# Performance work log

Hardware: AMD Instinct MI355X
Metric: run time of the kernel (lower is better)

The kernel has to match this reference:

```python
import jax, jax.numpy as jnp
import numpy as np

VOCAB, D_MODEL, D_STATE, D_CONV, EXPAND = 32000, 1024, 16, 4, 2
D_INNER = EXPAND * D_MODEL          # 2048
DT_RANK = (D_MODEL + 15) // 16      # 64
B, L = 2, 2048


def setup_inputs() -> dict:
    key = jax.random.key(0)
    ks = jax.random.split(key, 13)
    s = 0.02
    return {
        "tokens": jax.random.randint(ks[0], (B, L), 0, VOCAB, dtype=jnp.int32),
        "emb": jax.random.normal(ks[1], (VOCAB, D_MODEL), jnp.float32) * s,
        "in_proj_w": jax.random.normal(ks[2], (2 * D_INNER, D_MODEL), jnp.float32) * s,
        "conv_w": jax.random.normal(ks[3], (D_INNER, D_CONV), jnp.float32) * s,
        "conv_b": jnp.zeros((D_INNER,), jnp.float32),
        "x_proj_w": jax.random.normal(ks[4], (DT_RANK + 2 * D_STATE, D_INNER), jnp.float32) * s,
        "dt_proj_w": jax.random.normal(ks[5], (D_INNER, DT_RANK), jnp.float32) * s,
        "dt_proj_b": jax.random.normal(ks[6], (D_INNER,), jnp.float32) * 0.1,
        "A_log": jnp.log(jnp.broadcast_to(jnp.arange(1, D_STATE + 1, dtype=jnp.float32), (D_INNER, D_STATE))),
        "D": jnp.ones((D_INNER,), jnp.float32),
        "out_proj_w": jax.random.normal(ks[7], (D_MODEL, D_INNER), jnp.float32) * s,
        "head_w": jax.random.normal(ks[8], (VOCAB, D_MODEL), jnp.float32) * s,
        "head_b": jnp.zeros((VOCAB,), jnp.float32),
    }


def _silu(x):
    return x * jax.nn.sigmoid(x)


def _causal_dw_conv(x, w, b):
    # x: [B, L, D], w: [D, K] depthwise causal conv
    K = w.shape[1]
    Ln = x.shape[1]
    xp = jnp.pad(x, ((0, 0), (K - 1, 0), (0, 0)))
    out = b
    for k in range(K):
        out = out + xp[:, k:k + Ln, :] * w[:, k]
    return out


def _mamba_forward(tokens, emb, in_proj_w, conv_w, conv_b, x_proj_w,
                   dt_proj_w, dt_proj_b, A_log, D, out_proj_w, head_w, head_b):
    u = emb[tokens]                                        # [B, L, d_model]
    xz = jnp.einsum('bld,ed->ble', u, in_proj_w)           # [B, L, 2*d_inner]
    x, z = jnp.split(xz, 2, axis=-1)                       # each [B, L, d_inner]
    x = _silu(_causal_dw_conv(x, conv_w, conv_b))

    x_dbl = jnp.einsum('bld,ed->ble', x, x_proj_w)         # [B, L, dt_rank+2*d_state]
    dt, Bm, Cm = jnp.split(x_dbl, [DT_RANK, DT_RANK + D_STATE], axis=-1)
    dt = jax.nn.softplus(jnp.einsum('blr,dr->bld', dt, dt_proj_w) + dt_proj_b)  # [B, L, d_inner]

    A = -jnp.exp(A_log)                                    # [d_inner, d_state]

    # scan over time; per-step inputs in [L, B, ...] layout
    xs = (jnp.swapaxes(dt, 0, 1), jnp.swapaxes(Bm, 0, 1),
          jnp.swapaxes(Cm, 0, 1), jnp.swapaxes(x, 0, 1))

    def step(h, inp):
        dt_t, B_t, C_t, x_t = inp                          # [B,d_inner],[B,d_state],[B,d_state],[B,d_inner]
        dA = jnp.exp(dt_t[:, :, None] * A)                 # [B, d_inner, d_state]
        dBx = dt_t[:, :, None] * B_t[:, None, :] * x_t[:, :, None]
        h = dA * h + dBx
        y_t = jnp.einsum('bds,bs->bd', h, C_t)
        return h, y_t

    h0 = jnp.zeros((B, D_INNER, D_STATE), jnp.float32)
    _, ys = jax.lax.scan(step, h0, xs)                     # ys: [L, B, d_inner]
    y = jnp.swapaxes(ys, 0, 1) + D * x                     # [B, L, d_inner]
    y = y * _silu(z)
    out = jnp.einsum('ble,de->bld', y, out_proj_w)         # [B, L, d_model]
    logits = jnp.einsum('bld,vd->blv', out, head_w) + head_b
    return logits


def reference(tokens, emb, in_proj_w, conv_w, conv_b, x_proj_w,
              dt_proj_w, dt_proj_b, A_log, D, out_proj_w, head_w, head_b):
    return _mamba_forward(tokens, emb, in_proj_w, conv_w, conv_b, x_proj_w,
                          dt_proj_w, dt_proj_b, A_log, D, out_proj_w, head_w, head_b)
```

## Files before the change

kernel.cpp:

```cpp
#include <hip/hip_runtime.h>
#include <hip/hip_bf16.h>
#include <math.h>

#define LOG2E 1.44269504088896340736f

typedef __bf16 bf16x8 __attribute__((ext_vector_type(8)));
typedef float floatx4 __attribute__((ext_vector_type(4)));

static constexpr int VOCAB = 32000, D_MODEL = 1024, D_STATE = 16;
static constexpr int D_INNER = 2048, DT_RANK = 64, NB = 2, LSEQ = 2048;
static constexpr int NTOK = NB * LSEQ;
static constexpr int CL = 64, NCHUNK = LSEQ / CL;

__device__ __forceinline__ unsigned short f2bf(float f) {
    union { __hip_bfloat16 h; unsigned short u; } v;
    v.h = __float2bfloat16(f);
    return v.u;
}

__global__ void embed_kernel(const int* __restrict__ tok, const float* __restrict__ emb,
                             unsigned short* __restrict__ ubf) {
    int g = blockIdx.x * blockDim.x + threadIdx.x;
    int row = g >> 8;
    int c4 = (g & 255) * 4;
    if (row >= NTOK) return;
    int t = tok[row];
    float4 v = *(const float4*)(emb + (size_t)t * D_MODEL + c4);
    ushort4 o;
    o.x = f2bf(v.x); o.y = f2bf(v.y); o.z = f2bf(v.z); o.w = f2bf(v.w);
    *(ushort4*)(ubf + (size_t)row * D_MODEL + c4) = o;
}

__global__ void cvt_kernel(const float* __restrict__ in, unsigned short* __restrict__ out, int n4) {
    int g = blockIdx.x * blockDim.x + threadIdx.x;
    if (g >= n4) return;
    float4 v = ((const float4*)in)[g];
    ushort4 o;
    o.x = f2bf(v.x); o.y = f2bf(v.y); o.z = f2bf(v.z); o.w = f2bf(v.w);
    ((ushort4*)out)[g] = o;
}

__global__ void conv_silu_kernel(const float* __restrict__ xz, const float* __restrict__ cw,
                                 const float* __restrict__ cb, float* __restrict__ xf,
                                 unsigned short* __restrict__ xbf) {
    int g = blockIdx.x * blockDim.x + threadIdx.x;
    if (g >= NTOK * D_INNER) return;
    int d = g & (D_INNER - 1);
    int row = g >> 11;
    int l = row & (LSEQ - 1);
    float w0 = cw[d * 4 + 0], w1 = cw[d * 4 + 1], w2 = cw[d * 4 + 2], w3 = cw[d * 4 + 3];
    const float* xin = xz + (size_t)row * (2 * D_INNER) + d;
    const ptrdiff_t S = 2 * D_INNER;
    float acc = cb[d] + xin[0] * w3;
    if (l >= 1) acc += xin[-S] * w2;
    if (l >= 2) acc += xin[-2 * S] * w1;
    if (l >= 3) acc += xin[-3 * S] * w0;
    float sig = 1.f / (1.f + __builtin_amdgcn_exp2f(-acc * LOG2E));
    float v = acc * sig;
    xf[g] = v;
    xbf[g] = f2bf(v);
}

__global__ void dtin_kernel(const float* __restrict__ xdbl, unsigned short* __restrict__ dtin) {
    int g = blockIdx.x * blockDim.x + threadIdx.x;
    if (g >= NTOK * DT_RANK) return;
    int row = g >> 6, r = g & 63;
    dtin[g] = f2bf(xdbl[(size_t)row * 96 + r]);
}

__global__ void As_kernel(const float* __restrict__ A_log, float* __restrict__ As, int n) {
    int g = blockIdx.x * blockDim.x + threadIdx.x;
    if (g >= n) return;
    As[g] = -__builtin_amdgcn_exp2f(A_log[g] * LOG2E) * LOG2E;
}


__global__ void scan_part1(const float* __restrict__ dt, const float* __restrict__ x,
                           const float* __restrict__ xdbl, const float* __restrict__ As,
                           float* __restrict__ Pc, float* __restrict__ Hc) {
    int g = blockIdx.x * blockDim.x + threadIdx.x;
    int s = g & 15;
    int d = (g >> 4) & (D_INNER - 1);
    int c = (g >> 15) & (NCHUNK - 1);
    int b = g >> 20;
    float a2 = As[d * 16 + s];
    int row0 = b * LSEQ + c * CL;
    const float* dtp = dt + (size_t)row0 * D_INNER + d;
    const float* xp = x + (size_t)row0 * D_INNER + d;
    const float* bp = xdbl + (size_t)row0 * 96 + 64 + s;
    float h = 0.f, esum = 0.f;
    for (int l = 0; l < CL; ++l) {
        float dtv = dtp[(size_t)l * D_INNER];
        float xv = xp[(size_t)l * D_INNER];
        float Bv = bp[(size_t)l * 96];
        float e = dtv * a2;
        esum += e;
        float dA = __builtin_amdgcn_exp2f(e);
        h = dA * h + dtv * Bv * xv;
    }
    Pc[g] = __builtin_amdgcn_exp2f(esum);
    Hc[g] = h;
}

__global__ void scan_combine(const float* __restrict__ Pc, const float* __restrict__ Hc,
                             float* __restrict__ Hinit) {
    int g = blockIdx.x * blockDim.x + threadIdx.x;
    int ds = g & (D_INNER * D_STATE - 1);
    int b = g >> 15;
    size_t base = (size_t)b * NCHUNK * D_INNER * D_STATE + ds;
    float h = 0.f;
    for (int c = 0; c < NCHUNK; ++c) {
        size_t idx = base + (size_t)c * (D_INNER * D_STATE);
        Hinit[idx] = h;
        h = Pc[idx] * h + Hc[idx];
    }
}

__global__ void scan_part2(const float* __restrict__ dt, const float* __restrict__ x,
                           const float* __restrict__ xdbl, const float* __restrict__ xz,
                           const float* __restrict__ As, const float* __restrict__ Dvec,
                           const float* __restrict__ Hinit, unsigned short* __restrict__ ybf) {
    int g = blockIdx.x * blockDim.x + threadIdx.x;
    int s = g & 15;
    int d = (g >> 4) & (D_INNER - 1);
    int c = (g >> 15) & (NCHUNK - 1);
    int b = g >> 20;
    float a2 = As[d * 16 + s];
    float Dv = Dvec[d];
    int row0 = b * LSEQ + c * CL;
    const float* dtp = dt + (size_t)row0 * D_INNER + d;
    const float* xp = x + (size_t)row0 * D_INNER + d;
    const float* bp = xdbl + (size_t)row0 * 96 + 64 + s;
    const float* cp = xdbl + (size_t)row0 * 96 + 80 + s;
    const float* zp = xz + (size_t)row0 * 2 * D_INNER + D_INNER + d;
    unsigned short* yp = ybf + (size_t)row0 * D_INNER + d;
    float h = Hinit[g];
    for (int l = 0; l < CL; ++l) {
        float dtv = dtp[(size_t)l * D_INNER];
        float xv = xp[(size_t)l * D_INNER];
        float Bv = bp[(size_t)l * 96];
        float Cv = cp[(size_t)l * 96];
        float dA = __builtin_amdgcn_exp2f(dtv * a2);
        h = dA * h + dtv * Bv * xv;
        float p = h * Cv;
        p += __shfl_xor(p, 1);
        p += __shfl_xor(p, 2);
        p += __shfl_xor(p, 4);
        p += __shfl_xor(p, 8);
        if (s == 0) {
            float zv = zp[(size_t)l * 2 * D_INNER];
            float sig = 1.f / (1.f + __builtin_amdgcn_exp2f(-zv * LOG2E));
            float y = (p + Dv * xv) * (zv * sig);
            yp[(size_t)l * D_INNER] = f2bf(y);
        }
    }
}

__global__ __launch_bounds__(256, 2)
void gemm_bf16(const unsigned short* __restrict__ A, const unsigned short* __restrict__ Bw,
               float* __restrict__ Cf, unsigned short* __restrict__ Cb,
               const float* __restrict__ bias, int M, int N, int K, int epi) {
    constexpr int BM = 128, BN = 128, BK = 32, LDT = 40;
    __shared__ __align__(16) unsigned short lA[BM * LDT];
    __shared__ __align__(16) unsigned short lB[BN * LDT];
    int tid = threadIdx.x;
    int wave = tid >> 6, lane = tid & 63;
    int quad = lane >> 4, l16 = lane & 15;
    int wr = wave >> 1, wc = wave & 1;
    int m0 = blockIdx.y * BM, n0 = blockIdx.x * BN;

    floatx4 acc[4][4] = {};

    int r0 = tid >> 2, ch = tid & 3;
    int bn0 = n0 + r0; if (bn0 >= N) bn0 = N - 1;
    int bn1 = n0 + r0 + 64; if (bn1 >= N) bn1 = N - 1;
    const int nK = K / BK;
    for (int kt = 0; kt < nK; ++kt) {
        int k0 = kt * BK + ch * 8;
        uint4 va0 = *(const uint4*)(A + (size_t)(m0 + r0) * K + k0);
        uint4 va1 = *(const uint4*)(A + (size_t)(m0 + r0 + 64) * K + k0);
        uint4 vb0 = *(const uint4*)(Bw + (size_t)bn0 * K + k0);
        uint4 vb1 = *(const uint4*)(Bw + (size_t)bn1 * K + k0);
        __syncthreads();
        *(uint4*)&lA[r0 * LDT + ch * 8] = va0;
        *(uint4*)&lA[(r0 + 64) * LDT + ch * 8] = va1;
        *(uint4*)&lB[r0 * LDT + ch * 8] = vb0;
        *(uint4*)&lB[(r0 + 64) * LDT + ch * 8] = vb1;
        __syncthreads();
        bf16x8 af[4], bfr[4];
#pragma unroll
        for (int t = 0; t < 4; ++t) {
            af[t] = *(const bf16x8*)&lA[(wr * 64 + t * 16 + l16) * LDT + quad * 8];
            bfr[t] = *(const bf16x8*)&lB[(wc * 64 + t * 16 + l16) * LDT + quad * 8];
        }
#pragma unroll
        for (int mt = 0; mt < 4; ++mt)
#pragma unroll
            for (int nt = 0; nt < 4; ++nt)
                acc[mt][nt] = __builtin_amdgcn_mfma_f32_16x16x32_bf16(af[mt], bfr[nt], acc[mt][nt], 0, 0, 0);
    }
#pragma unroll
    for (int mt = 0; mt < 4; ++mt) {
#pragma unroll
        for (int nt = 0; nt < 4; ++nt) {
            int col = n0 + wc * 64 + nt * 16 + l16;
            if (col >= N) continue;
            float bv = (epi == 1 || epi == 2) ? bias[col] : 0.f;
#pragma unroll
            for (int r = 0; r < 4; ++r) {
                int row = m0 + wr * 64 + mt * 16 + quad * 4 + r;
                float v = acc[mt][nt][r] + bv;
                if (epi == 1) v = (v > 20.f) ? v : log1pf(__builtin_amdgcn_exp2f(v * LOG2E));
                if (epi == 3) Cb[(size_t)row * N + col] = f2bf(v);
                else Cf[(size_t)row * N + col] = v;
            }
        }
    }
}

extern "C" void kernel_launch(void* const* d_in, const int* in_sizes, int n_in,
                              void* d_out, int out_size, void* d_ws, size_t ws_size,
                              hipStream_t stream) {
    (void)in_sizes; (void)n_in; (void)out_size; (void)ws_size;
    const int* tokens = (const int*)d_in[0];
    const float* emb = (const float*)d_in[1];
    const float* in_proj_w = (const float*)d_in[2];
    const float* conv_w = (const float*)d_in[3];
    const float* conv_b = (const float*)d_in[4];
    const float* x_proj_w = (const float*)d_in[5];
    const float* dt_proj_w = (const float*)d_in[6];
    const float* dt_proj_b = (const float*)d_in[7];
    const float* A_log = (const float*)d_in[8];
    const float* Dvec = (const float*)d_in[9];
    const float* out_proj_w = (const float*)d_in[10];
    const float* head_w = (const float*)d_in[11];
    const float* head_b = (const float*)d_in[12];
    float* logits = (float*)d_out;

    char* ws = (char*)d_ws;
    size_t off = 0;
    auto alloc = [&](size_t bytes) -> void* {
        void* p = ws + off;
        off = (off + bytes + 255) & ~(size_t)255;
        return p;
    };
    unsigned short* u_bf = (unsigned short*)alloc((size_t)NTOK * D_MODEL * 2);
    unsigned short* Win_bf = (unsigned short*)alloc((size_t)2 * D_INNER * D_MODEL * 2);
    float* xz = (float*)alloc((size_t)NTOK * 2 * D_INNER * 4);
    float* xf = (float*)alloc((size_t)NTOK * D_INNER * 4);
    unsigned short* x_bf = (unsigned short*)alloc((size_t)NTOK * D_INNER * 2);
    unsigned short* Wxp_bf = (unsigned short*)alloc((size_t)96 * D_INNER * 2);
    float* xdbl = (float*)alloc((size_t)NTOK * 96 * 4);
    unsigned short* dtin_bf = (unsigned short*)alloc((size_t)NTOK * DT_RANK * 2);
    unsigned short* Wdt_bf = (unsigned short*)alloc((size_t)D_INNER * DT_RANK * 2);
    float* dtf = (float*)alloc((size_t)NTOK * D_INNER * 4);
    float* As = (float*)alloc((size_t)D_INNER * D_STATE * 4);
    unsigned short* y_bf = (unsigned short*)alloc((size_t)NTOK * D_INNER * 2);
    unsigned short* Wout_bf = (unsigned short*)alloc((size_t)D_MODEL * D_INNER * 2);
    unsigned short* out_bf = (unsigned short*)alloc((size_t)NTOK * D_MODEL * 2);
    float* Hinit = (float*)alloc((size_t)NB * NCHUNK * D_INNER * D_STATE * 4);
    unsigned short* Whead_bf = (unsigned short*)xz;
    float* Pc = (float*)u_bf;
    float* Hc = (float*)Win_bf;

    dim3 blk(256);

    embed_kernel<<<dim3(NTOK * D_MODEL / 4 / 256), blk, 0, stream>>>(tokens, emb, u_bf);
    cvt_kernel<<<dim3(2 * D_INNER * D_MODEL / 4 / 256), blk, 0, stream>>>(in_proj_w, Win_bf, 2 * D_INNER * D_MODEL / 4);
    gemm_bf16<<<dim3(2 * D_INNER / 128, NTOK / 128), blk, 0, stream>>>(
        u_bf, Win_bf, xz, nullptr, nullptr, NTOK, 2 * D_INNER, D_MODEL, 0);
    conv_silu_kernel<<<dim3(NTOK * D_INNER / 256), blk, 0, stream>>>(xz, conv_w, conv_b, xf, x_bf);
    cvt_kernel<<<dim3((96 * D_INNER / 4 + 255) / 256), blk, 0, stream>>>(x_proj_w, Wxp_bf, 96 * D_INNER / 4);
    gemm_bf16<<<dim3(1, NTOK / 128), blk, 0, stream>>>(
        x_bf, Wxp_bf, xdbl, nullptr, nullptr, NTOK, 96, D_INNER, 0);
    dtin_kernel<<<dim3(NTOK * DT_RANK / 256), blk, 0, stream>>>(xdbl, dtin_bf);
    cvt_kernel<<<dim3((D_INNER * DT_RANK / 4 + 255) / 256), blk, 0, stream>>>(dt_proj_w, Wdt_bf, D_INNER * DT_RANK / 4);
    gemm_bf16<<<dim3(D_INNER / 128, NTOK / 128), blk, 0, stream>>>(
        dtin_bf, Wdt_bf, dtf, nullptr, dt_proj_b, NTOK, D_INNER, DT_RANK, 1);
    As_kernel<<<dim3((D_INNER * D_STATE + 255) / 256), blk, 0, stream>>>(A_log, As, D_INNER * D_STATE);
    scan_part1<<<dim3(NB * NCHUNK * D_INNER * D_STATE / 256), blk, 0, stream>>>(
        dtf, xf, xdbl, As, Pc, Hc);
    scan_combine<<<dim3(NB * D_INNER * D_STATE / 256), blk, 0, stream>>>(Pc, Hc, Hinit);
    scan_part2<<<dim3(NB * NCHUNK * D_INNER * D_STATE / 256), blk, 0, stream>>>(
        dtf, xf, xdbl, xz, As, Dvec, Hinit, y_bf);
    cvt_kernel<<<dim3(D_MODEL * D_INNER / 4 / 256), blk, 0, stream>>>(out_proj_w, Wout_bf, D_MODEL * D_INNER / 4);
    gemm_bf16<<<dim3(D_MODEL / 128, NTOK / 128), blk, 0, stream>>>(
        y_bf, Wout_bf, nullptr, out_bf, nullptr, NTOK, D_MODEL, D_INNER, 3);
    cvt_kernel<<<dim3(VOCAB * D_MODEL / 4 / 256), blk, 0, stream>>>(head_w, Whead_bf, VOCAB * D_MODEL / 4);
    gemm_bf16<<<dim3(VOCAB / 128, NTOK / 128), blk, 0, stream>>>(
        out_bf, Whead_bf, logits, nullptr, head_b, NTOK, VOCAB, D_MODEL, 2);
}
```

Baseline: 1.543 ms.

## Use direct global-to-LDS loads and grouped tile ordering in bf16 GEMM

Replaces the register-staged global loads plus LDS stores with __builtin_amdgcn_global_load_lds 16-byte transfers straight into unpadded LDS tiles. It also remaps block indices into GROUP_M=8 swizzled groups to improve L2 reuse of the weight and activation tiles. The goal is to cut VGPR traffic and instruction count in the load path and to reduce DRAM refetches on the large vocab head GEMM. Dropping the LDS padding may add bank conflicts on fragment reads, and the loop is still single-buffered with two barriers per tile.

After: 1.507 ms. -2.3%, faster.

```diff
diff --git a/kernel.cpp b/kernel.cpp
--- a/kernel.cpp
+++ b/kernel.cpp
@@ -160,38 +160,57 @@
 void gemm_bf16(const unsigned short* __restrict__ A, const unsigned short* __restrict__ Bw,
                float* __restrict__ Cf, unsigned short* __restrict__ Cb,
                const float* __restrict__ bias, int M, int N, int K, int epi) {
-    constexpr int BM = 128, BN = 128, BK = 32, LDT = 40;
-    __shared__ __align__(16) unsigned short lA[BM * LDT];
-    __shared__ __align__(16) unsigned short lB[BN * LDT];
+    constexpr int BM = 128, BN = 128, BK = 32;
+    __shared__ __align__(16) unsigned short lA[BM * BK];
+    __shared__ __align__(16) unsigned short lB[BN * BK];
     int tid = threadIdx.x;
     int wave = tid >> 6, lane = tid & 63;
     int quad = lane >> 4, l16 = lane & 15;
     int wr = wave >> 1, wc = wave & 1;
-    int m0 = blockIdx.y * BM, n0 = blockIdx.x * BN;
+
+    int num_n = gridDim.x, num_m = gridDim.y;
+    int lin = blockIdx.y * num_n + blockIdx.x;
+    constexpr int GROUP_M = 8;
+    int gsize = GROUP_M * num_n;
+    int gid = lin / gsize;
+    int fm = gid * GROUP_M;
+    int gsz = (num_m - fm < GROUP_M) ? (num_m - fm) : GROUP_M;
+    int rem = lin - gid * gsize;
+    int m0 = (fm + rem % gsz) * BM;
+    int n0 = (rem / gsz) * BN;
 
     floatx4 acc[4][4] = {};
 
-    int r0 = tid >> 2, ch = tid & 3;
-    int bn0 = n0 + r0; if (bn0 >= N) bn0 = N - 1;
-    int bn1 = n0 + r0 + 64; if (bn1 >= N) bn1 = N - 1;
+    int crow = lane >> 2;
+    int ccol = (lane & 3) * 8;
+    int rA0 = m0 + wave * 16 + crow;
+    int rA1 = rA0 + 64;
+    int rB0 = n0 + wave * 16 + crow; if (rB0 >= N) rB0 = N - 1;
+    int rB1 = n0 + 64 + wave * 16 + crow; if (rB1 >= N) rB1 = N - 1;
+    const unsigned short* pA0 = A + (size_t)rA0 * K + ccol;
+    const unsigned short* pA1 = A + (size_t)rA1 * K + ccol;
+    const unsigned short* pB0 = Bw + (size_t)rB0 * K + ccol;
+    const unsigned short* pB1 = Bw + (size_t)rB1 * K + ccol;
+    typedef const __attribute__((address_space(1))) unsigned int gu32;
+    typedef __attribute__((address_space(3))) unsigned int lu32;
+    lu32* dA0 = (lu32*)(lA + wave * 512);
+    lu32* dA1 = (lu32*)(lA + (wave + 4) * 512);
+    lu32* dB0 = (lu32*)(lB + wave * 512);
+    lu32* dB1 = (lu32*)(lB + (wave + 4) * 512);
+
     const int nK = K / BK;
     for (int kt = 0; kt < nK; ++kt) {
-        int k0 = kt * BK + ch * 8;
-        uint4 va0 = *(const uint4*)(A + (size_t)(m0 + r0) * K + k0);
-        uint4 va1 = *(const uint4*)(A + (size_t)(m0 + r0 + 64) * K + k0);
-        uint4 vb0 = *(const uint4*)(Bw + (size_t)bn0 * K + k0);
-        uint4 vb1 = *(const uint4*)(Bw + (size_t)bn1 * K + k0);
         __syncthreads();
-        *(uint4*)&lA[r0 * LDT + ch * 8] = va0;
-        *(uint4*)&lA[(r0 + 64) * LDT + ch * 8] = va1;
-        *(uint4*)&lB[r0 * LDT + ch * 8] = vb0;
-        *(uint4*)&lB[(r0 + 64) * LDT + ch * 8] = vb1;
+        __builtin_amdgcn_global_load_lds((gu32*)(pA0 + kt * BK), dA0, 16, 0, 0);
+        __builtin_amdgcn_global_load_lds((gu32*)(pA1 + kt * BK), dA1, 16, 0, 0);
+        __builtin_amdgcn_global_load_lds((gu32*)(pB0 + kt * BK), dB0, 16, 0, 0);
+        __builtin_amdgcn_global_load_lds((gu32*)(pB1 + kt * BK), dB1, 16, 0, 0);
         __syncthreads();
         bf16x8 af[4], bfr[4];
 #pragma unroll
         for (int t = 0; t < 4; ++t) {
-            af[t] = *(const bf16x8*)&lA[(wr * 64 + t * 16 + l16) * LDT + quad * 8];
-            bfr[t] = *(const bf16x8*)&lB[(wc * 64 + t * 16 + l16) * LDT + quad * 8];
+            af[t] = *(const bf16x8*)&lA[(wr * 64 + t * 16 + l16) * BK + quad * 8];
+            bfr[t] = *(const bf16x8*)&lB[(wc * 64 + t * 16 + l16) * BK + quad * 8];
         }
 #pragma unroll
         for (int mt = 0; mt < 4; ++mt)
```
